# Performance work log

Hardware: AMD Instinct MI355X
Metric: run time of the kernel (lower is better)

## Reference

```python
import jax, jax.numpy as jnp
import numpy as np

BS, T, Q, HID, PROJ = 16, 16, 100, 256, 256


def setup_inputs() -> dict:
    key = jax.random.key(0)
    k1, k2, k3, k4, k5 = jax.random.split(key, 5)
    frame_embeds = jax.random.normal(k1, (BS, T, Q, HID), jnp.float32)
    other_frame_embeds = jax.random.normal(k2, (BS, T, Q, HID), jnp.float32)
    W = jax.random.normal(k3, (HID, PROJ), jnp.float32) / np.sqrt(HID).astype(np.float32)
    b = jax.random.normal(k4, (PROJ,), jnp.float32) * 0.01
    n = BS * Q
    mid = jax.random.randint(k5, (n, 1), 1, T - 1, dtype=jnp.int32)
    bridge = jnp.concatenate(
        [jnp.zeros((n, 1), jnp.int32), mid, jnp.full((n, 1), T - 1, jnp.int32)], axis=1
    )  # (n,3): head=0, random pivot in [1,T-2], tail=T-1
    return {"frame_embeds": frame_embeds, "other_frame_embeds": other_frame_embeds,
            "W": W, "b": b, "bridge": bridge}


def _prep(fe, W, b):
    # Linear proj, (bs,t,q,c)->(bs*q, t, c), L2-normalize per embedding.
    bs, t, q, _ = fe.shape
    x = fe @ W + b
    x = x.transpose(0, 2, 1, 3).reshape(bs * q, t, -1)
    return x / jnp.linalg.norm(x, axis=-1, keepdims=True)


def _forward(frame_embeds, other_frame_embeds, W, b, bridge, delta=0.3):
    cur = _prep(frame_embeds, W, b)      # (n,t,c)
    other = _prep(other_frame_embeds, W, b)
    bh = bridge[:, 0].astype(jnp.float32)
    bp_f = bridge[:, 1].astype(jnp.float32)
    bt = bridge[:, 2].astype(jnp.float32)
    alpha = (bp_f - bh) / (bt - bh)      # (n,)
    sigma = alpha * (bt - bp_f)          # (n,)
    g = jnp.take_along_axis(cur, bridge[:, :, None], axis=1)  # (n,3,c) head/pivot/tail
    # positive brownian-bridge distance
    x = g[:, 1] - (1.0 - alpha)[:, None] * g[:, 0] - alpha[:, None] * g[:, 2]
    numer = jnp.exp(-jnp.sum(x * x, axis=-1) / (2.0 * sigma ** 2))  # (n,)
    # negatives: pivot frame taken from every sequence in [cur; other].
    # ||m_ij - a_i||^2 = ||m_ij||^2 - 2 m_ij.a_i + ||a_i||^2 with m_ij = neg_all[j, bp_i],
    # avoiding the (n,N,3,c) repeat tensor of the original.
    neg_all = jnp.concatenate([cur, other], axis=0)            # (N,t,c)
    a = (1.0 - alpha)[:, None] * g[:, 0] + alpha[:, None] * g[:, 2]  # (n,c)
    cross = jnp.einsum('ic,jtc->ijt', a, neg_all)              # (n,N,t)
    bp = bridge[:, 1]
    cross_g = jnp.take_along_axis(cross, bp[:, None, None], axis=2)[..., 0]  # (n,N)
    nn2_g = jnp.sum(neg_all * neg_all, axis=-1).T[bp]          # (n,N)
    x2 = nn2_g - 2.0 * cross_g + jnp.sum(a * a, axis=-1)[:, None]
    dist = -x2 / (2.0 * sigma ** 2)[:, None]                   # (n,N)
    n = dist.shape[0]
    idx = jnp.arange(n)
    self_dist = dist[idx, idx]
    dist = dist.at[idx, idx].set(-10000.0)
    topv, _ = jax.lax.top_k(dist, 5)
    deno = jnp.exp(jnp.concatenate([self_dist[:, None], topv], axis=-1))  # (n,6)
    brownian_loss = (numer / deno.sum(axis=-1)).mean()
    score = jnp.einsum('nc,nc->n', cur[:, 0], cur[:, -1])
    head_tail_match = jax.nn.softplus(delta - score).mean()
    return brownian_loss, head_tail_match


def reference(frame_embeds, other_frame_embeds, W, b, bridge):
    return _forward(frame_embeds, other_frame_embeds, W, b, bridge)
```

## Files before the change

### kernel.cpp

```cpp
#include <hip/hip_runtime.h>
#include <hip/hip_bf16.h>

#define NROW 1600
#define NEG  3200
#define ROWS_FLAT 25600
#define NSPLIT 25

using bf16x8 = __attribute__((ext_vector_type(8))) short;
using f32x4  = __attribute__((ext_vector_type(4))) float;

__device__ __forceinline__ float bf2f(unsigned v) { return __uint_as_float(v << 16); }
__device__ __forceinline__ ushort f2bf(float f) {
  __hip_bfloat16 h = __float2bfloat16(f);
  return *(ushort*)&h;
}
__device__ __forceinline__ float load1(const ushort* p, size_t idx, int f32) {
  return f32 ? ((const float*)p)[idx] : bf2f(p[idx]);
}
__device__ __forceinline__ void load8(const ushort* p, size_t idx, int f32, float* o) {
  if (f32) {
    const float* q = (const float*)p;
    float4 a = *(const float4*)(q + idx);
    float4 b = *(const float4*)(q + idx + 4);
    o[0]=a.x; o[1]=a.y; o[2]=a.z; o[3]=a.w;
    o[4]=b.x; o[5]=b.y; o[6]=b.z; o[7]=b.w;
  } else {
    uint4 u = *(const uint4*)(p + idx);
    o[0]=bf2f(u.x & 0xffffu); o[1]=bf2f(u.x >> 16);
    o[2]=bf2f(u.y & 0xffffu); o[3]=bf2f(u.y >> 16);
    o[4]=bf2f(u.z & 0xffffu); o[5]=bf2f(u.z >> 16);
    o[6]=bf2f(u.w & 0xffffu); o[7]=bf2f(u.w >> 16);
  }
}
__device__ __forceinline__ int sniff_f32(const ushort* p, int lane) {
  unsigned e = ((unsigned)p[2*lane] >> 7) & 0xffu;
  unsigned long long b = __ballot(e >= 100u && e <= 140u);
  return (__popcll(b) >= 40) ? 0 : 1;
}

__global__ __launch_bounds__(256) void k_prep(const ushort* __restrict__ W,
    const ushort* __restrict__ fe0, const ushort* __restrict__ fe1,
    ushort* __restrict__ Wt, ushort* __restrict__ Xb, int* __restrict__ zbase) {
  const int tid = threadIdx.x;
  if (blockIdx.x == 0 && tid < 21) zbase[tid] = 0;
  if (blockIdx.x < 256) {
    int fW = sniff_f32(W, tid & 63);
    Wt[blockIdx.x * 256 + tid] = f2bf(load1(W, (size_t)tid * 256 + blockIdx.x, fW));
  }
  int r = blockIdx.x * 8 + (tid >> 5);
  int src1 = (r >= ROWS_FLAT);
  const ushort* src = src1 ? fe1 : fe0;
  size_t rr = (size_t)(src1 ? r - ROWS_FLAT : r);
  int f = sniff_f32(src, tid & 63);
  float o[8];
  load8(src, rr * 256 + (size_t)(tid & 31) * 8, f, o);
  uint4 u;
  u.x = (unsigned)f2bf(o[0]) | ((unsigned)f2bf(o[1]) << 16);
  u.y = (unsigned)f2bf(o[2]) | ((unsigned)f2bf(o[3]) << 16);
  u.z = (unsigned)f2bf(o[4]) | ((unsigned)f2bf(o[5]) << 16);
  u.w = (unsigned)f2bf(o[6]) | ((unsigned)f2bf(o[7]) << 16);
  *(uint4*)&Xb[(size_t)r * 256 + (tid & 31) * 8] = u;
}

__global__ __launch_bounds__(256) void k_proj(const ushort* __restrict__ Xb,
    const ushort* __restrict__ Wt, const ushort* __restrict__ bias,
    ushort* __restrict__ Pb) {
  __shared__ union {
    ushort x[64*256];
    ushort c[4][32*72];
  } sh;
  __shared__ float s_ss[4][64];
  const int tid = threadIdx.x;
  const int w = tid >> 6, lane = tid & 63, q = lane >> 4, m = lane & 15;
  const int grow0 = blockIdx.x * 64;
  const size_t rbase = (size_t)grow0 * 256;
  const int fB = sniff_f32(bias, lane);
  #pragma unroll
  for (int i = 0; i < 8; i++) {
    int c = w*8 + i;
    int r = 2*c + (lane >> 5);
    int kc = (lane & 31) ^ (r & 7);
    const ushort* gp = Xb + rbase + (size_t)r*256 + kc*8;
    __builtin_amdgcn_global_load_lds(
      (const __attribute__((address_space(1))) unsigned int*)gp,
      (__attribute__((address_space(3))) unsigned int*)&sh.x[c*512],
      16, 0, 0);
  }
  __syncthreads();
  f32x4 acc[4][4];
  #pragma unroll
  for (int nt = 0; nt < 4; nt++) {
    float bb = load1(bias, w*64 + nt*16 + m, fB);
    f32x4 v = {bb, bb, bb, bb};
    #pragma unroll
    for (int mt = 0; mt < 4; mt++) acc[mt][nt] = v;
  }
  const int sw = (m & 7) << 3;
  const ushort* wbase = Wt + (size_t)(w*64 + m)*256 + q*8;
  bf16x8 a_cur[4], b_cur[4];
  #pragma unroll
  for (int mt = 0; mt < 4; mt++)
    a_cur[mt] = *(const bf16x8*)&sh.x[(mt*16 + m)*256 + ((q*8) ^ sw)];
  #pragma unroll
  for (int nt = 0; nt < 4; nt++)
    b_cur[nt] = *(const bf16x8*)(wbase + (size_t)nt*16*256);
  #pragma unroll
  for (int k = 0; k < 8; k++) {
    bf16x8 a_nxt[4], b_nxt[4];
    if (k < 7) {
      int k0 = (k + 1) * 32;
      #pragma unroll
      for (int nt = 0; nt < 4; nt++)
        b_nxt[nt] = *(const bf16x8*)(wbase + (size_t)nt*16*256 + k0);
      int pk = (k0 + q*8) ^ sw;
      #pragma unroll
      for (int mt = 0; mt < 4; mt++)
        a_nxt[mt] = *(const bf16x8*)&sh.x[(mt*16 + m)*256 + pk];
    }
    #pragma unroll
    for (int nt = 0; nt < 4; nt++)
      #pragma unroll
      for (int mt = 0; mt < 4; mt++)
        acc[mt][nt] = __builtin_amdgcn_mfma_f32_16x16x32_bf16(a_cur[mt], b_cur[nt], acc[mt][nt], 0, 0, 0);
    if (k < 7) {
      #pragma unroll
      for (int x = 0; x < 4; x++) { a_cur[x] = a_nxt[x]; b_cur[x] = b_nxt[x]; }
    }
  }
  float ssp[4][4];
  #pragma unroll
  for (int mt = 0; mt < 4; mt++)
    #pragma unroll
    for (int reg = 0; reg < 4; reg++) {
      float s = 0.f;
      #pragma unroll
      for (int nt = 0; nt < 4; nt++) { float v = acc[mt][nt][reg]; s += v*v; }
      ssp[mt][reg] = s;
    }
  #pragma unroll
  for (int mk = 1; mk < 16; mk <<= 1)
    #pragma unroll
    for (int mt = 0; mt < 4; mt++)
      #pragma unroll
      for (int reg = 0; reg < 4; reg++) ssp[mt][reg] += __shfl_xor(ssp[mt][reg], mk, 64);
  if (m == 0)
    #pragma unroll
    for (int mt = 0; mt < 4; mt++)
      #pragma unroll
      for (int reg = 0; reg < 4; reg++) s_ss[w][mt*16 + 4*q + reg] = ssp[mt][reg];
  __syncthreads();
  float inv[4][4];
  #pragma unroll
  for (int mt = 0; mt < 4; mt++)
    #pragma unroll
    for (int reg = 0; reg < 4; reg++) {
      int row = mt*16 + 4*q + reg;
      float s = s_ss[0][row] + s_ss[1][row] + s_ss[2][row] + s_ss[3][row];
      inv[mt][reg] = 1.0f / sqrtf(s);
    }
  #pragma unroll
  for (int half = 0; half < 2; half++) {
    #pragma unroll
    for (int mt = half*2; mt < half*2 + 2; mt++)
      #pragma unroll
      for (int reg = 0; reg < 4; reg++) {
        int rl = (mt - half*2)*16 + 4*q + reg;
        #pragma unroll
        for (int nt = 0; nt < 4; nt++)
          sh.c[w][rl*72 + nt*16 + m] = f2bf(acc[mt][nt][reg] * inv[mt][reg]);
      }
    int rl = (lane >> 3), c16 = lane & 7;
    #pragma unroll
    for (int it = 0; it < 4; it++) {
      int row = it*8 + rl;
      int grow = grow0 + half*32 + row;
      int srcid = grow / ROWS_FLAT;
      int rem   = grow % ROWS_FLAT;
      int b  = rem / 1600;
      int t  = (rem / 100) & 15;
      int qq = rem % 100;
      size_t orow = ((size_t)(srcid*1600 + b*100 + qq) * 16 + t) * 256;
      uint4 v = *(uint4*)&sh.c[w][row*72 + c16*8];
      *(uint4*)(Pb + orow + w*64 + c16*8) = v;
    }
  }
}

__global__ __launch_bounds__(256) void k_bridge(const ushort* __restrict__ Pb,
    const int* __restrict__ bridge, ushort* __restrict__ Ab,
    float* __restrict__ prm, float* __restrict__ numer,
    int* __restrict__ cnt, int* __restrict__ lst, float* __restrict__ wsum) {
  int i = blockIdx.x, c = threadIdx.x;
  int bh = bridge[i*3+0], bp = bridge[i*3+1], bt = bridge[i*3+2];
  float bhf = (float)bh, bpf = (float)bp, btf = (float)bt;
  float alpha = (bpf - bhf) / (btf - bhf);
  float sigma = alpha * (btf - bpf);
  const ushort* base = Pb + (size_t)i * 16 * 256;
  float g0 = bf2f(base[bh*256 + c]), g1 = bf2f(base[bp*256 + c]), g2 = bf2f(base[bt*256 + c]);
  float head = bf2f(base[c]), tail = bf2f(base[15*256 + c]);
  float a = (1.0f - alpha) * g0 + alpha * g2;
  float x = g1 - a;
  Ab[(size_t)i*256 + c] = f2bf(a);
  float xx = x*x, aac = a*a, sc = head*tail;
  #pragma unroll
  for (int mk = 1; mk < 64; mk <<= 1) {
    xx  += __shfl_xor(xx, mk, 64);
    aac += __shfl_xor(aac, mk, 64);
    sc  += __shfl_xor(sc, mk, 64);
  }
  __shared__ float red[3][4];
  int wv = c >> 6;
  if ((c & 63) == 0) { red[0][wv]=xx; red[1][wv]=aac; red[2][wv]=sc; }
  __syncthreads();
  if (c == 0) {
    float XX = red[0][0]+red[0][1]+red[0][2]+red[0][3];
    float AA = red[1][0]+red[1][1]+red[1][2]+red[1][3];
    float SC = red[2][0]+red[2][1]+red[2][2]+red[2][3];
    float inv2s2 = 1.0f / (2.0f * sigma * sigma);
    prm[i*2+0] = inv2s2;
    prm[i*2+1] = AA;
    numer[i] = expf(-XX * inv2s2);
    float sp = log1pf(expf(0.3f - SC));
    atomicAdd(wsum + 1, sp * (1.0f / 1600.0f));
    int pos = atomicAdd(cnt + bp, 1);
    lst[bp * 1600 + pos] = i;
  }
}

__device__ __forceinline__ void sort5(float* c) {
  #define CE(i,j) { float hi = fmaxf(c[i], c[j]), lo = fminf(c[i], c[j]); c[i]=hi; c[j]=lo; }
  CE(0,1) CE(3,4) CE(2,4) CE(2,3) CE(1,4) CE(0,3) CE(0,2) CE(1,3) CE(1,2)
  #undef CE
}
__device__ __forceinline__ void ins5(float* t, float v) {
  float hi, lo;
  hi = fmaxf(t[0], v); lo = fminf(t[0], v); t[0] = hi; v = lo;
  hi = fmaxf(t[1], v); lo = fminf(t[1], v); t[1] = hi; v = lo;
  hi = fmaxf(t[2], v); lo = fminf(t[2], v); t[2] = hi; v = lo;
  hi = fmaxf(t[3], v); lo = fminf(t[3], v); t[3] = hi; v = lo;
  t[4] = fmaxf(t[4], v);
}

__global__ __launch_bounds__(256) void k_cross(const ushort* __restrict__ Pb,
    const ushort* __restrict__ Ab, const float* __restrict__ prm,
    const int* __restrict__ cnt, const int* __restrict__ lst,
    float* __restrict__ part) {
  int t = blockIdx.z;
  int n_t = min(cnt[t], 1600);
  int i0 = blockIdx.y * 64;
  if (i0 >= n_t) return;
  int j0 = blockIdx.x * 128;
  __shared__ int s_gis[64];
  __shared__ float s_red[4][64][6];
  int tid = threadIdx.x;
  if (tid < 64) {
    int gi = lst[t*1600 + min(i0 + tid, n_t - 1)];
    s_gis[tid] = min(max(gi, 0), NROW - 1);
  }
  __syncthreads();
  const int w = tid >> 6, lane = tid & 63, q = lane >> 4, m = lane & 15;
  const ushort* jp0 = Pb + ((size_t)(j0 + w*32 + m)*16 + t) * 256 + q*8;
  const ushort* jp1 = jp0 + (size_t)16*16*256;
  int gi[4];
  const ushort* ip[4];
  #pragma unroll
  for (int it = 0; it < 4; it++) {
    gi[it] = s_gis[it*16 + m];
    ip[it] = Ab + (size_t)gi[it] * 256 + q*8;
  }
  f32x4 acc[2][4];
  #pragma unroll
  for (int jt = 0; jt < 2; jt++)
    #pragma unroll
    for (int it = 0; it < 4; it++) { f32x4 z = {0.f,0.f,0.f,0.f}; acc[jt][it] = z; }
  bf16x8 jc0 = *(const bf16x8*)(jp0);
  bf16x8 jc1 = *(const bf16x8*)(jp1);
  bf16x8 ic[4];
  #pragma unroll
  for (int it = 0; it < 4; it++) ic[it] = *(const bf16x8*)(ip[it]);
  #pragma unroll
  for (int k = 0; k < 8; k++) {
    bf16x8 jn0, jn1, in[4];
    if (k < 7) {
      int o = (k + 1) * 32;
      jn0 = *(const bf16x8*)(jp0 + o);
      jn1 = *(const bf16x8*)(jp1 + o);
      #pragma unroll
      for (int it = 0; it < 4; it++) in[it] = *(const bf16x8*)(ip[it] + o);
    }
    #pragma unroll
    for (int it = 0; it < 4; it++) {
      acc[0][it] = __builtin_amdgcn_mfma_f32_16x16x32_bf16(jc0, ic[it], acc[0][it], 0, 0, 0);
      acc[1][it] = __builtin_amdgcn_mfma_f32_16x16x32_bf16(jc1, ic[it], acc[1][it], 0, 0, 0);
    }
    if (k < 7) { jc0 = jn0; jc1 = jn1;
      #pragma unroll
      for (int it = 0; it < 4; it++) ic[it] = in[it];
    }
  }
  float top[4][5], selfv[4];
  float pi[4], pa[4];
  #pragma unroll
  for (int it = 0; it < 4; it++) {
    pi[it] = prm[gi[it]*2]; pa[it] = prm[gi[it]*2+1];
    selfv[it] = -1e30f;
    #pragma unroll
    for (int k = 0; k < 5; k++) top[it][k] = -1e30f;
  }
  #pragma unroll
  for (int jt = 0; jt < 2; jt++)
    #pragma unroll
    for (int reg = 0; reg < 4; reg++) {
      int j = j0 + w*32 + jt*16 + 4*q + reg;
      #pragma unroll
      for (int it = 0; it < 4; it++) {
        float d = -(1.0f - 2.0f*acc[jt][it][reg] + pa[it]) * pi[it];
        if (j == gi[it]) selfv[it] = d; else ins5(top[it], d);
      }
    }
  #pragma unroll
  for (int mk = 16; mk <= 32; mk <<= 1) {
    #pragma unroll
    for (int it = 0; it < 4; it++) {
      float o[5], c[5];
      #pragma unroll
      for (int k = 0; k < 5; k++) o[k] = __shfl_xor(top[it][k], mk, 64);
      #pragma unroll
      for (int k = 0; k < 5; k++) c[k] = fmaxf(top[it][k], o[4 - k]);
      sort5(c);
      #pragma unroll
      for (int k = 0; k < 5; k++) top[it][k] = c[k];
      selfv[it] = fmaxf(selfv[it], __shfl_xor(selfv[it], mk, 64));
    }
  }
  if (q == 0) {
    #pragma unroll
    for (int it = 0; it < 4; it++) {
      #pragma unroll
      for (int k = 0; k < 5; k++) s_red[w][it*16 + m][k] = top[it][k];
      s_red[w][it*16 + m][5] = selfv[it];
    }
  }
  __syncthreads();
  if (tid < 64 && i0 + tid < n_t) {
    float T[5], S = s_red[0][tid][5];
    #pragma unroll
    for (int k = 0; k < 5; k++) T[k] = s_red[0][tid][k];
    #pragma unroll
    for (int w2 = 1; w2 < 4; w2++) {
      #pragma unroll
      for (int k = 0; k < 5; k++) ins5(T, s_red[w2][tid][k]);
      S = fmaxf(S, s_red[w2][tid][5]);
    }
    float* pp = part + ((size_t)s_gis[tid]*NSPLIT + blockIdx.x) * 6;
    #pragma unroll
    for (int k = 0; k < 5; k++) pp[k] = T[k];
    pp[5] = S;
  }
}

__global__ __launch_bounds__(64) void k_merge(const float* __restrict__ part,
    const float* __restrict__ numer, float* __restrict__ wsum, int* __restrict__ done,
    const ushort* __restrict__ fe0, void* __restrict__ out) {
  int i = blockIdx.x * 64 + threadIdx.x;
  const float* pp = part + (size_t)i * NSPLIT * 6;
  float T[5]; float S = pp[5];
  #pragma unroll
  for (int k = 0; k < 5; k++) T[k] = pp[k];
  #pragma unroll
  for (int s = 1; s < NSPLIT; s++) {
    const float* ps = pp + s*6;
    float v0 = ps[0], v1 = ps[1], v2 = ps[2], v3 = ps[3], v4 = ps[4], v5 = ps[5];
    ins5(T, v0); ins5(T, v1); ins5(T, v2); ins5(T, v3); ins5(T, v4);
    S = fmaxf(S, v5);
  }
  float deno = expf(S);
  #pragma unroll
  for (int k = 0; k < 5; k++) deno += expf(T[k]);
  float local = numer[i] / deno;
  #pragma unroll
  for (int mk = 1; mk < 64; mk <<= 1) local += __shfl_xor(local, mk, 64);
  __shared__ int s_last;
  if (threadIdx.x == 0) {
    atomicAdd(wsum + 0, local * (1.0f / 1600.0f));
    __threadfence();
    s_last = (atomicAdd(done, 1) == 24);
  }
  __syncthreads();
  if (s_last) {
    int f = sniff_f32(fe0, threadIdx.x);
    if (threadIdx.x == 0) {
      __threadfence();
      float brown = __hip_atomic_load(wsum + 0, __ATOMIC_RELAXED, __HIP_MEMORY_SCOPE_AGENT);
      float sp    = __hip_atomic_load(wsum + 1, __ATOMIC_RELAXED, __HIP_MEMORY_SCOPE_AGENT);
      if (f) {
        ((float*)out)[0] = brown;
        ((float*)out)[1] = sp;
      } else {
        ushort* o = (ushort*)out;
        o[0] = f2bf(brown);
        o[1] = f2bf(sp);
      }
    }
  }
}

extern "C" void kernel_launch(void* const* d_in, const int* in_sizes, int n_in,
                              void* d_out, int out_size, void* d_ws, size_t ws_size,
                              hipStream_t stream) {
  const ushort* fe0    = (const ushort*)d_in[0];
  const ushort* fe1    = (const ushort*)d_in[1];
  const ushort* W      = (const ushort*)d_in[2];
  const ushort* bias   = (const ushort*)d_in[3];
  const int*    bridge = (const int*)d_in[4];

  ushort* Pb    = (ushort*)d_ws;
  ushort* Xb    = Pb + 13107200;
  ushort* Ab    = Xb + 13107200;
  ushort* Wt    = Ab + 409600;
  float*  part  = (float*)(Wt + 65536);
  float*  prm   = part + 240000;
  float*  numer = prm + 3200;
  float*  wsum  = numer + 1600;
  int*    cnt   = (int*)(wsum + 4);
  int*    done  = cnt + 16;
  int*    lst   = done + 1;

  k_prep  <<<6400, 256, 0, stream>>>(W, fe0, fe1, Wt, Xb, (int*)wsum);
  k_proj  <<<800, 256, 0, stream>>>(Xb, Wt, bias, Pb);
  k_bridge<<<1600, 256, 0, stream>>>(Pb, bridge, Ab, prm, numer, cnt, lst, wsum);
  k_cross <<<dim3(NSPLIT, 7, 16), 256, 0, stream>>>(Pb, Ab, prm, cnt, lst, part);
  k_merge <<<25, 64, 0, stream>>>(part, numer, wsum, done, fe0, d_out);
}
```

Measured before the change: 198.4 us.

## Fuse bridge computation into projection kernel and reorder projected layout t-major

The input rows are now permuted in the prep kernel so each projection block holds 4 whole sequences (16 frames each). The separate bridge kernel is folded into the projection epilogue, which reads head, pivot and tail straight from shared memory, saving a launch and a global re-read of the projected tensor. The projected output is stored as (t, N, c), so the cross kernel's per-pivot loads become contiguous. It also adds s_setprio around the MFMA block. The cost is an extra barrier and reduction work in half of the projection blocks.

```diff
diff --git a/kernel.cpp b/kernel.cpp
--- a/kernel.cpp
+++ b/kernel.cpp
@@ -50,31 +50,42 @@
   int r = blockIdx.x * 8 + (tid >> 5);
   int src1 = (r >= ROWS_FLAT);
   const ushort* src = src1 ? fe1 : fe0;
-  size_t rr = (size_t)(src1 ? r - ROWS_FLAT : r);
+  int rr = src1 ? r - ROWS_FLAT : r;
   int f = sniff_f32(src, tid & 63);
   float o[8];
-  load8(src, rr * 256 + (size_t)(tid & 31) * 8, f, o);
+  load8(src, (size_t)rr * 256 + (size_t)(tid & 31) * 8, f, o);
+  int b  = rr / 1600;
+  int rm = rr - b * 1600;
+  int t  = rm / 100;
+  int q  = rm - t * 100;
+  int I  = src1 * 1600 + b * 100 + q;
   uint4 u;
   u.x = (unsigned)f2bf(o[0]) | ((unsigned)f2bf(o[1]) << 16);
   u.y = (unsigned)f2bf(o[2]) | ((unsigned)f2bf(o[3]) << 16);
   u.z = (unsigned)f2bf(o[4]) | ((unsigned)f2bf(o[5]) << 16);
   u.w = (unsigned)f2bf(o[6]) | ((unsigned)f2bf(o[7]) << 16);
-  *(uint4*)&Xb[(size_t)r * 256 + (tid & 31) * 8] = u;
+  *(uint4*)&Xb[((size_t)I * 16 + t) * 256 + (size_t)(tid & 31) * 8] = u;
 }
 
 __global__ __launch_bounds__(256) void k_proj(const ushort* __restrict__ Xb,
     const ushort* __restrict__ Wt, const ushort* __restrict__ bias,
-    ushort* __restrict__ Pb) {
+    const int* __restrict__ bridge, ushort* __restrict__ Pb,
+    ushort* __restrict__ Ab, float* __restrict__ prm, float* __restrict__ numer,
+    int* __restrict__ cnt, int* __restrict__ lst, float* __restrict__ wsum) {
   __shared__ union {
     ushort x[64*256];
     ushort c[4][32*72];
   } sh;
   __shared__ float s_ss[4][64];
+  __shared__ float s_bb[2][4][2][3];
+  __shared__ int   s_brg[4][3];
   const int tid = threadIdx.x;
   const int w = tid >> 6, lane = tid & 63, q = lane >> 4, m = lane & 15;
   const int grow0 = blockIdx.x * 64;
+  const int hasB = (blockIdx.x < 400);
   const size_t rbase = (size_t)grow0 * 256;
   const int fB = sniff_f32(bias, lane);
+  if (hasB && tid < 12) s_brg[tid / 3][tid % 3] = bridge[(blockIdx.x * 4 + tid / 3) * 3 + tid % 3];
   #pragma unroll
   for (int i = 0; i < 8; i++) {
     int c = w*8 + i;
@@ -173,57 +184,58 @@
     #pragma unroll
     for (int it = 0; it < 4; it++) {
       int row = it*8 + rl;
-      int grow = grow0 + half*32 + row;
-      int srcid = grow / ROWS_FLAT;
-      int rem   = grow % ROWS_FLAT;
-      int b  = rem / 1600;
-      int t  = (rem / 100) & 15;
-      int qq = rem % 100;
-      size_t orow = ((size_t)(srcid*1600 + b*100 + qq) * 16 + t) * 256;
+      int r   = half*32 + row;
+      int ig  = r >> 4, t = r & 15;
+      int I   = blockIdx.x*4 + ig;
+      size_t orow = ((size_t)t * NEG + I) * 256;
       uint4 v = *(uint4*)&sh.c[w][row*72 + c16*8];
       *(uint4*)(Pb + orow + w*64 + c16*8) = v;
     }
-  }
-}
-
-__global__ __launch_bounds__(256) void k_bridge(const ushort* __restrict__ Pb,
-    const int* __restrict__ bridge, ushort* __restrict__ Ab,
-    float* __restrict__ prm, float* __restrict__ numer,
-    int* __restrict__ cnt, int* __restrict__ lst, float* __restrict__ wsum) {
-  int i = blockIdx.x, c = threadIdx.x;
-  int bh = bridge[i*3+0], bp = bridge[i*3+1], bt = bridge[i*3+2];
-  float bhf = (float)bh, bpf = (float)bp, btf = (float)bt;
-  float alpha = (bpf - bhf) / (btf - bhf);
-  float sigma = alpha * (btf - bpf);
-  const ushort* base = Pb + (size_t)i * 16 * 256;
-  float g0 = bf2f(base[bh*256 + c]), g1 = bf2f(base[bp*256 + c]), g2 = bf2f(base[bt*256 + c]);
-  float head = bf2f(base[c]), tail = bf2f(base[15*256 + c]);
-  float a = (1.0f - alpha) * g0 + alpha * g2;
-  float x = g1 - a;
-  Ab[(size_t)i*256 + c] = f2bf(a);
-  float xx = x*x, aac = a*a, sc = head*tail;
-  #pragma unroll
-  for (int mk = 1; mk < 64; mk <<= 1) {
-    xx  += __shfl_xor(xx, mk, 64);
-    aac += __shfl_xor(aac, mk, 64);
-    sc  += __shfl_xor(sc, mk, 64);
-  }
-  __shared__ float red[3][4];
-  int wv = c >> 6;
-  if ((c & 63) == 0) { red[0][wv]=xx; red[1][wv]=aac; red[2][wv]=sc; }
-  __syncthreads();
-  if (c == 0) {
-    float XX = red[0][0]+red[0][1]+red[0][2]+red[0][3];
-    float AA = red[1][0]+red[1][1]+red[1][2]+red[1][3];
-    float SC = red[2][0]+red[2][1]+red[2][2]+red[2][3];
-    float inv2s2 = 1.0f / (2.0f * sigma * sigma);
-    prm[i*2+0] = inv2s2;
-    prm[i*2+1] = AA;
-    numer[i] = expf(-XX * inv2s2);
-    float sp = log1pf(expf(0.3f - SC));
-    atomicAdd(wsum + 1, sp * (1.0f / 1600.0f));
-    int pos = atomicAdd(cnt + bp, 1);
-    lst[bp * 1600 + pos] = i;
+    if (hasB) {
+      #pragma unroll
+      for (int ih = 0; ih < 2; ih++) {
+        int ig = half*2 + ih;
+        int bh = s_brg[ig][0], bp = s_brg[ig][1], bt = s_brg[ig][2];
+        float alpha = ((float)bp - (float)bh) / ((float)bt - (float)bh);
+        int rb = ih*16;
+        float g0 = bf2f(sh.c[w][(rb + bh)*72 + lane]);
+        float g1 = bf2f(sh.c[w][(rb + bp)*72 + lane]);
+        float g2 = bf2f(sh.c[w][(rb + bt)*72 + lane]);
+        float hd = bf2f(sh.c[w][(rb +  0)*72 + lane]);
+        float tl = bf2f(sh.c[w][(rb + 15)*72 + lane]);
+        float a = (1.0f - alpha) * g0 + alpha * g2;
+        float x = g1 - a;
+        int I = blockIdx.x*4 + ig;
+        Ab[(size_t)I*256 + w*64 + lane] = f2bf(a);
+        float xx = x*x, aa = a*a, sc = hd*tl;
+        #pragma unroll
+        for (int mk = 1; mk < 64; mk <<= 1) {
+          xx += __shfl_xor(xx, mk, 64);
+          aa += __shfl_xor(aa, mk, 64);
+          sc += __shfl_xor(sc, mk, 64);
+        }
+        if (lane == 0) { s_bb[half][w][ih][0] = xx; s_bb[half][w][ih][1] = aa; s_bb[half][w][ih][2] = sc; }
+      }
+      __syncthreads();
+      if (tid < 2) {
+        int ig = half*2 + tid;
+        int I = blockIdx.x*4 + ig;
+        float XX = s_bb[half][0][tid][0] + s_bb[half][1][tid][0] + s_bb[half][2][tid][0] + s_bb[half][3][tid][0];
+        float AA = s_bb[half][0][tid][1] + s_bb[half][1][tid][1] + s_bb[half][2][tid][1] + s_bb[half][3][tid][1];
+        float SC = s_bb[half][0][tid][2] + s_bb[half][1][tid][2] + s_bb[half][2][tid][2] + s_bb[half][3][tid][2];
+        int bh = s_brg[ig][0], bp = s_brg[ig][1], bt = s_brg[ig][2];
+        float alpha = ((float)bp - (float)bh) / ((float)bt - (float)bh);
+        float sigma = alpha * ((float)bt - (float)bp);
+        float inv2s2 = 1.0f / (2.0f * sigma * sigma);
+        prm[I*2+0] = inv2s2;
+        prm[I*2+1] = AA;
+        numer[I] = expf(-XX * inv2s2);
+        float sp = log1pf(expf(0.3f - SC));
+        atomicAdd(wsum + 1, sp * (1.0f / 1600.0f));
+        int pos = atomicAdd(cnt + bp, 1);
+        lst[bp * 1600 + pos] = I;
+      }
+    }
   }
 }
 
@@ -259,8 +271,8 @@
   }
   __syncthreads();
   const int w = tid >> 6, lane = tid & 63, q = lane >> 4, m = lane & 15;
-  const ushort* jp0 = Pb + ((size_t)(j0 + w*32 + m)*16 + t) * 256 + q*8;
-  const ushort* jp1 = jp0 + (size_t)16*16*256;
+  const ushort* jp0 = Pb + ((size_t)t * NEG + (j0 + w*32 + m)) * 256 + q*8;
+  const ushort* jp1 = jp0 + (size_t)16*256;
   int gi[4];
   const ushort* ip[4];
   #pragma unroll
@@ -288,11 +300,13 @@
       #pragma unroll
       for (int it = 0; it < 4; it++) in[it] = *(const bf16x8*)(ip[it] + o);
     }
+    __builtin_amdgcn_s_setprio(1);
     #pragma unroll
     for (int it = 0; it < 4; it++) {
       acc[0][it] = __builtin_amdgcn_mfma_f32_16x16x32_bf16(jc0, ic[it], acc[0][it], 0, 0, 0);
       acc[1][it] = __builtin_amdgcn_mfma_f32_16x16x32_bf16(jc1, ic[it], acc[1][it], 0, 0, 0);
     }
+    __builtin_amdgcn_s_setprio(0);
     if (k < 7) { jc0 = jn0; jc1 = jn1;
       #pragma unroll
       for (int it = 0; it < 4; it++) ic[it] = in[it];
@@ -427,8 +441,7 @@
   int*    lst   = done + 1;
 
   k_prep  <<<6400, 256, 0, stream>>>(W, fe0, fe1, Wt, Xb, (int*)wsum);
-  k_proj  <<<800, 256, 0, stream>>>(Xb, Wt, bias, Pb);
-  k_bridge<<<1600, 256, 0, stream>>>(Pb, bridge, Ab, prm, numer, cnt, lst, wsum);
+  k_proj  <<<800, 256, 0, stream>>>(Xb, Wt, bias, bridge, Pb, Ab, prm, numer, cnt, lst, wsum);
   k_cross <<<dim3(NSPLIT, 7, 16), 256, 0, stream>>>(Pb, Ab, prm, cnt, lst, part);
   k_merge <<<25, 64, 0, stream>>>(part, numer, wsum, done, fe0, d_out);
 }
```

New measurement: 176.0 us. 11.3% less time.
